# Kernel optimization log

Hardware: AMD Instinct MI355X
Metric: run time of the kernel (lower is better)

Reference implementation:

```python
import jax, jax.numpy as jnp
import numpy as np

N = 50000      # nodes per graph batch (per side)
E = 600000     # edges per side
B = 4096       # number of graphs (drug pairs)
D = 128        # node_dim == hidden_dim
K = 128        # kge_dim
R = 86         # rel_total
L = 3          # n_iter
EPS = 1e-5


def setup_inputs() -> dict:
    key = jax.random.key(0)
    ks = jax.random.split(key, 16)
    inp = {}
    inp["x1"] = jax.random.normal(ks[0], (N, D), jnp.float32)
    inp["x2"] = jax.random.normal(ks[1], (N, D), jnp.float32)
    inp["edge_index1"] = jax.random.randint(ks[2], (2, E), 0, N)
    inp["edge_index2"] = jax.random.randint(ks[3], (2, E), 0, N)
    inp["batch1"] = jnp.sort(jax.random.randint(ks[4], (N,), 0, B))
    inp["batch2"] = jnp.sort(jax.random.randint(ks[5], (N,), 0, B))
    inp["rel"] = jax.random.randint(ks[6], (B,), 0, R)
    # SAGEConv params, stacked over L layers (all [D,D] since node_dim==hidden_dim)
    sc = 0.05
    inp["Wl"] = jax.random.normal(ks[7], (L, D, D), jnp.float32) * sc   # lin on aggregated neighbors (has bias)
    inp["bl"] = jnp.zeros((L, D), jnp.float32)
    inp["Wr"] = jax.random.normal(ks[8], (L, D, D), jnp.float32) * sc   # root (self) lin, no bias
    # BatchNorm (eval mode: running stats)
    inp["bn_gamma"] = jnp.ones((L, D), jnp.float32)
    inp["bn_beta"] = jnp.zeros((L, D), jnp.float32)
    inp["bn_mean"] = jnp.zeros((L, D), jnp.float32)
    inp["bn_var"] = jnp.ones((L, D), jnp.float32)
    # relation embedding + final MLP
    inp["kge"] = jax.random.normal(ks[9], (R, K), jnp.float32)
    inp["W1"] = jax.random.normal(ks[10], (2 * D + K, D), jnp.float32) * sc
    inp["b1"] = jnp.zeros((D,), jnp.float32)
    inp["W2"] = jax.random.normal(ks[11], (D, 1), jnp.float32) * sc
    inp["b2"] = jnp.zeros((1,), jnp.float32)
    return inp


def _gnn(x, edge_index, Wl, bl, Wr, g, b, m, v):
    src, dst = edge_index[0], edge_index[1]
    deg = jax.ops.segment_sum(jnp.ones((E,), x.dtype), dst, num_segments=N)
    deg = jnp.maximum(deg, 1.0)[:, None]
    for i in range(L):
        agg = jax.ops.segment_sum(x[src], dst, num_segments=N) / deg  # mean aggregation
        h = agg @ Wl[i] + bl[i] + x @ Wr[i]                           # SAGEConv
        h = (h - m[i]) * (g[i] / jnp.sqrt(v[i] + EPS)) + b[i]         # BN (eval)
        x = jax.nn.relu(h)                                            # dropout = identity (eval)
    return x


def reference(x1, edge_index1, batch1, x2, edge_index2, batch2, rel,
              Wl, bl, Wr, bn_gamma, bn_beta, bn_mean, bn_var,
              kge, W1, b1, W2, b2):
    h1 = _gnn(x1, edge_index1, Wl, bl, Wr, bn_gamma, bn_beta, bn_mean, bn_var)
    h2 = _gnn(x2, edge_index2, Wl, bl, Wr, bn_gamma, bn_beta, bn_mean, bn_var)
    p1 = jax.ops.segment_sum(h1, batch1, num_segments=B)  # global_add_pool
    p2 = jax.ops.segment_sum(h2, batch2, num_segments=B)
    r = kge[rel]                                          # [B, K]
    z = jnp.concatenate([p1, p2, r], axis=-1)             # [B, 2D+K]
    h = jax.nn.relu(z @ W1 + b1)
    out = h @ W2 + b2
    return out.reshape(-1)
```

## Files before the change

### kernel.cpp

```cpp
#include <hip/hip_runtime.h>

#define NN 50000
#define NE 600000
#define NB 4096
#define DD 128
#define EPSV 1e-5f
#define NBKT 196
#define NCHUNK 256
#define CHSZ ((NE + NCHUNK - 1) / NCHUNK)

typedef __bf16 bf16x8 __attribute__((ext_vector_type(8)));
typedef float f32x4 __attribute__((ext_vector_type(4)));
typedef float f32x2 __attribute__((ext_vector_type(2)));

__device__ inline unsigned short f2bf(float f) {
    unsigned u = __float_as_uint(f);
    u = (u + 0x7FFFu + ((u >> 16) & 1u)) >> 16;
    return (unsigned short)u;
}
__device__ inline float bf2f(unsigned short h) {
    return __uint_as_float(((unsigned)h) << 16);
}

__global__ void k_prep(const float* __restrict__ x1, const float* __restrict__ x2,
                       unsigned short* __restrict__ xh, unsigned short* __restrict__ xl,
                       const float* __restrict__ Wl, const float* __restrict__ Wr,
                       const float* __restrict__ W1,
                       unsigned short* __restrict__ wfp, unsigned* __restrict__ w1p,
                       const int* __restrict__ d0, const int* __restrict__ d1,
                       int* __restrict__ bcnt) {
    __shared__ int h[NBKT];
    int b = blockIdx.x;
    int tid = threadIdx.x;
    if (b < 12500) {
        int i = b * 256 + tid;
        const float* x = (i < NN * 32) ? x1 : x2;
        int j = (i < NN * 32) ? i : i - NN * 32;
        float4 v = ((const float4*)x)[j];
        ushort4 hh, ll;
        hh.x = f2bf(v.x); ll.x = f2bf(v.x - bf2f(hh.x));
        hh.y = f2bf(v.y); ll.y = f2bf(v.y - bf2f(hh.y));
        hh.z = f2bf(v.z); ll.z = f2bf(v.z - bf2f(hh.z));
        hh.w = f2bf(v.w); ll.w = f2bf(v.w - bf2f(hh.w));
        ((ushort4*)xh)[i] = hh;
        ((ushort4*)xl)[i] = ll;
    } else if (b < 12500 + 576) {
        int t = (b - 12500) * 256 + tid;
        if (t < 3 * 128 * 256) {
            int k = t & 255;
            int n = (t >> 8) & 127;
            int l = t >> 15;
            float w = (k < 128) ? Wl[l * 16384 + k * 128 + n] : Wr[l * 16384 + (k - 128) * 128 + n];
            unsigned short hh = f2bf(w);
            unsigned short lo = f2bf(w - bf2f(hh));
            int c = k >> 5, kk = k & 31;
            size_t base = (size_t)l * 65536 + (size_t)c * 8192 + n * 32 + kk;
            wfp[base] = hh;
            wfp[base + 4096] = lo;
        } else if (t < 3 * 128 * 256 + 128 * 384) {
            int u = t - 3 * 128 * 256;
            int n = u / 384;
            int k = u - n * 384;
            float w = W1[k * 128 + n];
            unsigned short hh = f2bf(w);
            unsigned short ll = f2bf(w - bf2f(hh));
            w1p[u] = ((unsigned)hh << 16) | (unsigned)ll;
        }
    } else {
        int hb = b - 13076;
        int side = (hb >= NCHUNK) ? 1 : 0;
        int c = hb - side * NCHUNK;
        const int* dst = side ? d1 : d0;
        for (int i = tid; i < NBKT; i += 256) h[i] = 0;
        __syncthreads();
        int e0 = c * CHSZ, e1 = min(e0 + CHSZ, NE);
        for (int e = e0 + tid; e < e1; e += 256) atomicAdd(&h[dst[e] >> 8], 1);
        __syncthreads();
        int* bc = bcnt + ((size_t)side * NCHUNK + c) * NBKT;
        for (int i = tid; i < NBKT; i += 256) bc[i] = h[i];
    }
}

__global__ void k_s1(int* __restrict__ bcnt, int* __restrict__ btot) {
    int side = (blockIdx.x >= NBKT) ? 1 : 0;
    int b = blockIdx.x - side * NBKT;
    int tid = threadIdx.x;
    int idx = ((size_t)side * NCHUNK + tid) * NBKT + b;
    int v = bcnt[idx];
    int lane = tid & 63, wv = tid >> 6;
    int x = v;
#pragma unroll
    for (int off = 1; off < 64; off <<= 1) {
        int y = __shfl_up(x, off, 64);
        if (lane >= off) x += y;
    }
    __shared__ int ws4[4];
    if (lane == 63) ws4[wv] = x;
    __syncthreads();
    int add = 0;
#pragma unroll
    for (int w = 0; w < 4; w++)
        if (w < wv) add += ws4[w];
    int incl = x + add;
    bcnt[idx] = incl - v;
    if (tid == 255) btot[side * NBKT + b] = incl;
}

__global__ void k_s2(const int* __restrict__ btot, int* __restrict__ bbase,
                     int* __restrict__ ptrC) {
    int side = blockIdx.x;
    int tid = threadIdx.x;
    int v = (tid < NBKT) ? btot[side * NBKT + tid] : 0;
    int lane = tid & 63, wv = tid >> 6;
    int x = v;
#pragma unroll
    for (int off = 1; off < 64; off <<= 1) {
        int y = __shfl_up(x, off, 64);
        if (lane >= off) x += y;
    }
    __shared__ int ws4[4];
    if (lane == 63) ws4[wv] = x;
    __syncthreads();
    int add = 0;
#pragma unroll
    for (int w = 0; w < 4; w++)
        if (w < wv) add += ws4[w];
    int incl = x + add;
    if (tid < NBKT) bbase[side * NBKT + tid] = incl - v;
    if (tid == 0 && side == 1) ptrC[2 * NN] = 2 * NE;
}

__global__ void k_part(const int* __restrict__ s0, const int* __restrict__ d0,
                       const int* __restrict__ s1, const int* __restrict__ d1,
                       const int* __restrict__ bcnt, const int* __restrict__ bbase,
                       int* __restrict__ part) {
    int side = (blockIdx.x >= NCHUNK) ? 1 : 0;
    int c = blockIdx.x - side * NCHUNK;
    const int* src = side ? s1 : s0;
    const int* dst = side ? d1 : d0;
    int tid = threadIdx.x;
    __shared__ int off[NBKT];
    const int* bc = bcnt + ((size_t)side * NCHUNK + c) * NBKT;
    for (int i = tid; i < NBKT; i += 256) off[i] = bbase[side * NBKT + i] + bc[i];
    __syncthreads();
    int e0 = c * CHSZ, e1 = min(e0 + CHSZ, NE);
    int* P = part + (size_t)side * NE;
    int soff = side * NN;
    for (int e = e0 + tid; e < e1; e += 256) {
        int d = dst[e];
        int pos = atomicAdd(&off[d >> 8], 1);
        P[pos] = ((src[e] + soff) << 8) | (d & 255);
    }
}

__global__ void k_csr(const int* __restrict__ part, const int* __restrict__ bbase,
                      int* __restrict__ ptrC, float* __restrict__ invdC,
                      int* __restrict__ csrC) {
    int side = (blockIdx.x >= NBKT) ? 1 : 0;
    int b = blockIdx.x - side * NBKT;
    int tid = threadIdx.x;
    const int* P = part + (size_t)side * NE;
    int base = bbase[side * NBKT + b];
    int endp = (b == NBKT - 1) ? NE : bbase[side * NBKT + b + 1];
    __shared__ int cnt[256];
    cnt[tid] = 0;
    __syncthreads();
    for (int e = base + tid; e < endp; e += 256) atomicAdd(&cnt[P[e] & 255], 1);
    __syncthreads();
    int v = cnt[tid];
    int lane = tid & 63, wv = tid >> 6;
    int x = v;
#pragma unroll
    for (int off = 1; off < 64; off <<= 1) {
        int y = __shfl_up(x, off, 64);
        if (lane >= off) x += y;
    }
    __shared__ int ws4[4];
    if (lane == 63) ws4[wv] = x;
    __syncthreads();
    int add = 0;
#pragma unroll
    for (int w = 0; w < 4; w++)
        if (w < wv) add += ws4[w];
    int excl = x + add - v;
    int node = (b << 8) + tid;
    if (node < NN) {
        ptrC[side * NN + node] = side * NE + base + excl;
        invdC[side * NN + node] = 1.0f / (float)(v > 1 ? v : 1);
    }
    __syncthreads();
    cnt[tid] = excl;
    __syncthreads();
    for (int e = base + tid; e < endp; e += 256) {
        int p = P[e];
        int pos = atomicAdd(&cnt[p & 255], 1);
        csrC[(size_t)side * NE + base + pos] = p >> 8;
    }
}

__global__ void k_gather(const unsigned short* __restrict__ xh, const int* __restrict__ ptr,
                         const int* __restrict__ csr, const float* __restrict__ invd,
                         unsigned short* __restrict__ aggH) {
    int wid = threadIdx.x >> 6;
    int lane = threadIdx.x & 63;
    int q = lane >> 4;
    int c = lane & 15;
    int n = blockIdx.x * 4 + wid;
    if (n >= 2 * NN) return;
    int beg = ptr[n], end = ptr[n + 1];
    float id = invd[n];
    f32x2 a2[4];
#pragma unroll
    for (int k = 0; k < 4; k++) a2[k] = (f32x2){0.f, 0.f};

    for (int base = beg; base < end; base += 64) {
        int cnt = min(end - base, 64);
        int idxv = csr[base + min(lane, cnt - 1)];
        for (int e0 = 0; e0 < cnt; e0 += 8) {
            int eA = e0 + q;
            int eB = e0 + 4 + q;
            int iA = __shfl(idxv, eA, 64);
            int iB = __shfl(idxv, eB, 64);
            f32x2 wA2 = (eA < cnt) ? (f32x2){1.f, 1.f} : (f32x2){0.f, 0.f};
            f32x2 wB2 = (eB < cnt) ? (f32x2){1.f, 1.f} : (f32x2){0.f, 0.f};
            uint4 vA = *(const uint4*)(xh + (((unsigned)iA << 7) + (c << 3)));
            uint4 vB = *(const uint4*)(xh + (((unsigned)iB << 7) + (c << 3)));
            a2[0] += wA2 * (f32x2){__uint_as_float(vA.x << 16), __uint_as_float(vA.x & 0xffff0000u)};
            a2[1] += wA2 * (f32x2){__uint_as_float(vA.y << 16), __uint_as_float(vA.y & 0xffff0000u)};
            a2[2] += wA2 * (f32x2){__uint_as_float(vA.z << 16), __uint_as_float(vA.z & 0xffff0000u)};
            a2[3] += wA2 * (f32x2){__uint_as_float(vA.w << 16), __uint_as_float(vA.w & 0xffff0000u)};
            a2[0] += wB2 * (f32x2){__uint_as_float(vB.x << 16), __uint_as_float(vB.x & 0xffff0000u)};
            a2[1] += wB2 * (f32x2){__uint_as_float(vB.y << 16), __uint_as_float(vB.y & 0xffff0000u)};
            a2[2] += wB2 * (f32x2){__uint_as_float(vB.z << 16), __uint_as_float(vB.z & 0xffff0000u)};
            a2[3] += wB2 * (f32x2){__uint_as_float(vB.w << 16), __uint_as_float(vB.w & 0xffff0000u)};
        }
    }
    float a[8];
    a[0] = a2[0][0]; a[1] = a2[0][1];
    a[2] = a2[1][0]; a[3] = a2[1][1];
    a[4] = a2[2][0]; a[5] = a2[2][1];
    a[6] = a2[3][0]; a[7] = a2[3][1];
#pragma unroll
    for (int k = 0; k < 8; k++) {
        a[k] += __shfl_xor(a[k], 16, 64);
        a[k] += __shfl_xor(a[k], 32, 64);
    }
    if (q == 0) {
        unsigned short h0 = f2bf(a[0] * id), h1 = f2bf(a[1] * id);
        unsigned short h2 = f2bf(a[2] * id), h3 = f2bf(a[3] * id);
        unsigned short h4 = f2bf(a[4] * id), h5 = f2bf(a[5] * id);
        unsigned short h6 = f2bf(a[6] * id), h7 = f2bf(a[7] * id);
        uint4 o;
        o.x = (unsigned)h0 | ((unsigned)h1 << 16);
        o.y = (unsigned)h2 | ((unsigned)h3 << 16);
        o.z = (unsigned)h4 | ((unsigned)h5 << 16);
        o.w = (unsigned)h6 | ((unsigned)h7 << 16);
        *(uint4*)(aggH + (size_t)n * DD + c * 8) = o;
    }
}

__launch_bounds__(256)
__global__ void k_gemmL(const unsigned short* __restrict__ AH,
                        const unsigned short* __restrict__ XH, const unsigned short* __restrict__ XL,
                        const unsigned short* __restrict__ wfp,
                        const float* __restrict__ bl, const float* __restrict__ g,
                        const float* __restrict__ be, const float* __restrict__ mn,
                        const float* __restrict__ vr,
                        unsigned short* __restrict__ OH, unsigned short* __restrict__ OL,
                        float* __restrict__ Of, int f32out) {
    __shared__ __align__(16) unsigned short sA[2][128 * 32];
    __shared__ __align__(16) unsigned short sW[2][128 * 32];
    int tid = threadIdx.x;
    int lane = tid & 63, w = tid >> 6;
    int fm = lane & 15, kq = lane >> 4;
    int m0 = blockIdx.x * 128;
    int wr = (w & 1) * 64;
    int wn = (w >> 1) * 64;
    int ksw = kq ^ ((fm >> 1) & 3);

    int ldsoff[2], sfull[2];
    size_t gbase[2];
    bool sok[2];
#pragma unroll
    for (int i = 0; i < 2; i++) {
        int s = tid + 256 * i;
        int row = s >> 2, seg = s & 3;
        sfull[i] = s;
        ldsoff[i] = row * 32 + (seg ^ ((row >> 1) & 3)) * 8;
        int grow = m0 + row;
        sok[i] = grow < 2 * NN;
        gbase[i] = (size_t)grow * DD + seg * 8;
    }

    uint4 ph[2], plr[2], pwh[2], pwl[2];
#pragma unroll
    for (int i = 0; i < 2; i++) {
        ph[i] = sok[i] ? *(const uint4*)(AH + gbase[i]) : make_uint4(0, 0, 0, 0);
        pwh[i] = *(const uint4*)(wfp + sfull[i] * 8);
        pwl[i] = *(const uint4*)(wfp + 4096 + sfull[i] * 8);
    }

    float scv[4], shv[4];
#pragma unroll
    for (int nt = 0; nt < 4; nt++) {
        int jj = wn + nt * 16 + fm;
        float s = g[jj] * rsqrtf(vr[jj] + EPSV);
        scv[nt] = s;
        shv[nt] = (bl[jj] - mn[jj]) * s + be[jj];
    }

    f32x4 acc[4][4];
#pragma unroll
    for (int i = 0; i < 4; i++)
#pragma unroll
        for (int j = 0; j < 4; j++) acc[i][j] = (f32x4){0.f, 0.f, 0.f, 0.f};

#pragma unroll
    for (int c = 0; c < 8; c++) {
        int isA = (c < 4);
        if (c > 0) __syncthreads();
#pragma unroll
        for (int i = 0; i < 2; i++) {
            *(uint4*)&sA[0][ldsoff[i]] = ph[i];
            if (!isA) *(uint4*)&sA[1][ldsoff[i]] = plr[i];
            *(uint4*)&sW[0][ldsoff[i]] = pwh[i];
            *(uint4*)&sW[1][ldsoff[i]] = pwl[i];
        }
        if (c < 7) {
            int cn = c + 1;
            const unsigned short* SH = (cn < 4) ? AH : XH;
            size_t koff = (size_t)(cn & 3) * 32;
            const unsigned short* wbn = wfp + (size_t)cn * 8192;
#pragma unroll
            for (int i = 0; i < 2; i++) {
                ph[i] = sok[i] ? *(const uint4*)(SH + gbase[i] + koff) : make_uint4(0, 0, 0, 0);
                if (cn >= 4)
                    plr[i] = sok[i] ? *(const uint4*)(XL + gbase[i] + koff) : make_uint4(0, 0, 0, 0);
                pwh[i] = *(const uint4*)(wbn + sfull[i] * 8);
                pwl[i] = *(const uint4*)(wbn + 4096 + sfull[i] * 8);
            }
        }
        __syncthreads();

        bf16x8 ah[4], al[4];
#pragma unroll
        for (int mt = 0; mt < 4; mt++) {
            int r = wr + mt * 16 + fm;
            ah[mt] = *(const bf16x8*)&sA[0][r * 32 + ksw * 8];
            if (!isA) al[mt] = *(const bf16x8*)&sA[1][r * 32 + ksw * 8];
        }
#pragma unroll
        for (int nt = 0; nt < 4; nt++) {
            int nr = wn + nt * 16 + fm;
            bf16x8 wh = *(const bf16x8*)&sW[0][nr * 32 + ksw * 8];
            bf16x8 wl = *(const bf16x8*)&sW[1][nr * 32 + ksw * 8];
#pragma unroll
            for (int mt = 0; mt < 4; mt++) {
                acc[mt][nt] = __builtin_amdgcn_mfma_f32_16x16x32_bf16(ah[mt], wh, acc[mt][nt], 0, 0, 0);
                acc[mt][nt] = __builtin_amdgcn_mfma_f32_16x16x32_bf16(ah[mt], wl, acc[mt][nt], 0, 0, 0);
                if (!isA)
                    acc[mt][nt] = __builtin_amdgcn_mfma_f32_16x16x32_bf16(al[mt], wh, acc[mt][nt], 0, 0, 0);
            }
        }
    }

#pragma unroll
    for (int mt = 0; mt < 4; mt++) {
#pragma unroll
        for (int r = 0; r < 4; r++) {
            int grow = m0 + wr + mt * 16 + kq * 4 + r;
            if (grow < 2 * NN) {
#pragma unroll
                for (int nt = 0; nt < 4; nt++) {
                    int gcol = wn + nt * 16 + fm;
                    float o = fmaxf(acc[mt][nt][r] * scv[nt] + shv[nt], 0.f);
                    if (f32out) {
                        Of[(size_t)grow * DD + gcol] = o;
                    } else {
                        unsigned short h = f2bf(o);
                        OH[(size_t)grow * DD + gcol] = h;
                        OL[(size_t)grow * DD + gcol] = f2bf(o - bf2f(h));
                    }
                }
            }
        }
    }
}

__launch_bounds__(128)
__global__ void k_pool2z(const float* __restrict__ cf, const int* __restrict__ bt1,
                         const int* __restrict__ bt2, const int* __restrict__ rel,
                         const float* __restrict__ kge,
                         unsigned short* __restrict__ zh, unsigned short* __restrict__ zl) {
    int side = (blockIdx.x >= NB) ? 1 : 0;
    int b = blockIdx.x - side * NB;
    const int* batch = side ? bt2 : bt1;
    const float* h = cf + (size_t)side * NN * DD;
    __shared__ int sr[2];
    if (threadIdx.x < 2) {
        int target = b + (int)threadIdx.x;
        int lo = 0, hi = NN;
        while (lo < hi) {
            int mid = (lo + hi) >> 1;
            if (batch[mid] < target) lo = mid + 1; else hi = mid;
        }
        sr[threadIdx.x] = lo;
    }
    __syncthreads();
    int beg = sr[0], end = sr[1];
    int t = threadIdx.x;
    float acc = 0.f;
    for (int r = beg; r < end; r++) acc += h[(size_t)r * DD + t];
    size_t zo = (size_t)b * 384 + side * 128 + t;
    unsigned short hh = f2bf(acc);
    zh[zo] = hh;
    zl[zo] = f2bf(acc - bf2f(hh));
    if (side == 0) {
        float kv = kge[(size_t)rel[b] * 128 + t];
        size_t zk = (size_t)b * 384 + 256 + t;
        unsigned short kh = f2bf(kv);
        zh[zk] = kh;
        zl[zk] = f2bf(kv - bf2f(kh));
    }
}

__launch_bounds__(256)
__global__ void k_mlp2(const unsigned short* __restrict__ zh, const unsigned short* __restrict__ zl,
                       const unsigned* __restrict__ w1p,
                       const float* __restrict__ b1, const float* __restrict__ W2,
                       const float* __restrict__ b2, float* __restrict__ out) {
    __shared__ __align__(16) unsigned short sZ[2][32 * 40];
    __shared__ __align__(16) unsigned short sW[2][128 * 40];
    __shared__ float hpart[32][4];
    int tid = threadIdx.x;
    int m0 = blockIdx.x * 32;
    int lane = tid & 63, w = tid >> 6;
    int fm = lane & 15, q = lane >> 4;
    int wn = w * 32;

    f32x4 acc[2][2];
#pragma unroll
    for (int i = 0; i < 2; i++)
#pragma unroll
        for (int j = 0; j < 2; j++) acc[i][j] = (f32x4){0.f, 0.f, 0.f, 0.f};

    for (int c = 0; c < 12; c++) {
        int k0 = c * 32;
        __syncthreads();
        {
            int row = tid >> 3, seg = tid & 7;
            size_t off = (size_t)(m0 + row) * 384 + k0 + seg * 4;
            *(ushort4*)&sZ[0][row * 40 + seg * 4] = *(const ushort4*)(zh + off);
            *(ushort4*)&sZ[1][row * 40 + seg * 4] = *(const ushort4*)(zl + off);
        }
#pragma unroll
        for (int i = 0; i < 4; i++) {
            int u = tid + 256 * i;
            int row = u >> 3, seg = u & 7;
            uint4 val = *(const uint4*)(w1p + (size_t)row * 384 + k0 + seg * 4);
            ushort4 hi, lo;
            hi.x = val.x >> 16; hi.y = val.y >> 16; hi.z = val.z >> 16; hi.w = val.w >> 16;
            lo.x = val.x & 0xFFFF; lo.y = val.y & 0xFFFF; lo.z = val.z & 0xFFFF; lo.w = val.w & 0xFFFF;
            *(ushort4*)&sW[0][row * 40 + seg * 4] = hi;
            *(ushort4*)&sW[1][row * 40 + seg * 4] = lo;
        }
        __syncthreads();
        bf16x8 zfh[2], zfl[2];
#pragma unroll
        for (int mt = 0; mt < 2; mt++) {
            int r = mt * 16 + fm;
            zfh[mt] = *(const bf16x8*)&sZ[0][r * 40 + q * 8];
            zfl[mt] = *(const bf16x8*)&sZ[1][r * 40 + q * 8];
        }
#pragma unroll
        for (int nt = 0; nt < 2; nt++) {
            int nr = wn + nt * 16 + fm;
            bf16x8 wh = *(const bf16x8*)&sW[0][nr * 40 + q * 8];
            bf16x8 wl = *(const bf16x8*)&sW[1][nr * 40 + q * 8];
#pragma unroll
            for (int mt = 0; mt < 2; mt++) {
                acc[mt][nt] = __builtin_amdgcn_mfma_f32_16x16x32_bf16(zfh[mt], wh, acc[mt][nt], 0, 0, 0);
                acc[mt][nt] = __builtin_amdgcn_mfma_f32_16x16x32_bf16(zfh[mt], wl, acc[mt][nt], 0, 0, 0);
                acc[mt][nt] = __builtin_amdgcn_mfma_f32_16x16x32_bf16(zfl[mt], wh, acc[mt][nt], 0, 0, 0);
            }
        }
    }

    float b1v[2], w2v[2];
#pragma unroll
    for (int nt = 0; nt < 2; nt++) {
        int col = wn + nt * 16 + fm;
        b1v[nt] = b1[col];
        w2v[nt] = W2[col];
    }
#pragma unroll
    for (int mt = 0; mt < 2; mt++) {
#pragma unroll
        for (int r = 0; r < 4; r++) {
            float val = 0.f;
#pragma unroll
            for (int nt = 0; nt < 2; nt++)
                val += fmaxf(acc[mt][nt][r] + b1v[nt], 0.f) * w2v[nt];
#pragma unroll
            for (int m = 1; m < 16; m <<= 1) val += __shfl_xor(val, m, 64);
            if (fm == 0) hpart[mt * 16 + q * 4 + r][w] = val;
        }
    }
    __syncthreads();
    if (tid < 32)
        out[m0 + tid] = hpart[tid][0] + hpart[tid][1] + hpart[tid][2] + hpart[tid][3] + b2[0];
}

extern "C" void kernel_launch(void* const* d_in, const int* in_sizes, int n_in,
                              void* d_out, int out_size, void* d_ws, size_t ws_size,
                              hipStream_t stream) {
    const float* x1  = (const float*)d_in[0];
    const float* x2  = (const float*)d_in[1];
    const int*   ei1 = (const int*)d_in[2];
    const int*   ei2 = (const int*)d_in[3];
    const int*   bt1 = (const int*)d_in[4];
    const int*   bt2 = (const int*)d_in[5];
    const int*   rel = (const int*)d_in[6];
    const float* Wl  = (const float*)d_in[7];
    const float* bl  = (const float*)d_in[8];
    const float* Wr  = (const float*)d_in[9];
    const float* g   = (const float*)d_in[10];
    const float* be  = (const float*)d_in[11];
    const float* mn  = (const float*)d_in[12];
    const float* vr  = (const float*)d_in[13];
    const float* kge = (const float*)d_in[14];
    const float* W1  = (const float*)d_in[15];
    const float* b1v = (const float*)d_in[16];
    const float* W2  = (const float*)d_in[17];
    const float* b2v = (const float*)d_in[18];

    char* ws = (char*)d_ws;
    size_t off = 0;
    auto alloc = [&](size_t bytes) {
        void* p = ws + off;
        off += (bytes + 255) & ~(size_t)255;
        return p;
    };
    const size_t PL = (size_t)2 * NN * DD;
    unsigned short* xbufH = (unsigned short*)alloc(PL * 2);
    unsigned short* xbufL = (unsigned short*)alloc(PL * 2);
    unsigned short* obufH = (unsigned short*)alloc(PL * 2);
    unsigned short* obufL = (unsigned short*)alloc(PL * 2);
    unsigned short* aggH  = (unsigned short*)alloc(PL * 2);
    unsigned short* wfp   = (unsigned short*)alloc((size_t)3 * 65536 * 2);
    unsigned* w1p  = (unsigned*)alloc((size_t)128 * 384 * 4);
    unsigned short* zh = (unsigned short*)alloc((size_t)NB * 384 * 2);
    unsigned short* zl = (unsigned short*)alloc((size_t)NB * 384 * 2);
    int*   bcnt    = (int*)alloc((size_t)2 * NCHUNK * NBKT * 4);
    int*   btot    = (int*)alloc((size_t)2 * NBKT * 4);
    int*   bbase   = (int*)alloc((size_t)2 * NBKT * 4);
    int*   part    = (int*)alloc((size_t)2 * NE * 4);
    int*   ptrC    = (int*)alloc((size_t)(2 * NN + 1) * 4);
    float* invdC   = (float*)alloc((size_t)2 * NN * 4);
    int*   csrC    = (int*)alloc((size_t)2 * NE * 4);
    if (off > ws_size) return;

    float* cf = (float*)obufH;

    const int nbPrep  = 12500 + 576 + 512;
    const int nbNode4 = (2 * NN + 3) / 4;
    const int nbGemmL = (2 * NN + 127) / 128;

    k_prep<<<nbPrep, 256, 0, stream>>>(x1, x2, xbufH, xbufL, Wl, Wr, W1, wfp, w1p,
                                       ei1 + NE, ei2 + NE, bcnt);

    k_s1<<<2 * NBKT, 256, 0, stream>>>(bcnt, btot);
    k_s2<<<2, 256, 0, stream>>>(btot, bbase, ptrC);
    k_part<<<2 * NCHUNK, 256, 0, stream>>>(ei1, ei1 + NE, ei2, ei2 + NE, bcnt, bbase, part);
    k_csr<<<2 * NBKT, 256, 0, stream>>>(part, bbase, ptrC, invdC, csrC);

    k_gather<<<nbNode4, 256, 0, stream>>>(xbufH, ptrC, csrC, invdC, aggH);
    k_gemmL<<<nbGemmL, 256, 0, stream>>>(aggH, xbufH, xbufL, wfp, bl, g, be, mn, vr,
                                         obufH, obufL, (float*)nullptr, 0);
    k_gather<<<nbNode4, 256, 0, stream>>>(obufH, ptrC, csrC, invdC, aggH);
    k_gemmL<<<nbGemmL, 256, 0, stream>>>(aggH, obufH, obufL, wfp + 65536, bl + 128, g + 128,
                                         be + 128, mn + 128, vr + 128,
                                         xbufH, xbufL, (float*)nullptr, 0);
    k_gather<<<nbNode4, 256, 0, stream>>>(xbufH, ptrC, csrC, invdC, aggH);
    k_gemmL<<<nbGemmL, 256, 0, stream>>>(aggH, xbufH, xbufL, wfp + 131072, bl + 256, g + 256,
                                         be + 256, mn + 256, vr + 256,
                                         (unsigned short*)nullptr, (unsigned short*)nullptr, cf, 1);

    k_pool2z<<<2 * NB, 128, 0, stream>>>(cf, bt1, bt2, rel, kge, zh, zl);
    k_mlp2<<<NB / 32, 256, 0, stream>>>(zh, zl, w1p, b1v, W2, b2v, (float*)d_out);
}
```

Before: 493.7 us.

## Stage GEMM epilogue through LDS for coalesced stores; drop register prefetch

The GEMM epilogue now writes the activated results into shared memory in two halves and then stores them to global memory as 16-byte coalesced vectors, instead of scattered 2-byte or 4-byte per-lane stores. The bf16 hi/lo pair is packed into one word in LDS and split when it is written out. The register-level prefetch of the next K-chunk is also removed, and the K loop is no longer unrolled. Loads now happen right before the LDS stores, which lowers register pressure but loses the overlap of global loads with the MFMA work.

```diff
diff --git a/kernel.cpp b/kernel.cpp
--- a/kernel.cpp
+++ b/kernel.cpp
@@ -268,8 +268,9 @@
                         const float* __restrict__ vr,
                         unsigned short* __restrict__ OH, unsigned short* __restrict__ OL,
                         float* __restrict__ Of, int f32out) {
-    __shared__ __align__(16) unsigned short sA[2][128 * 32];
-    __shared__ __align__(16) unsigned short sW[2][128 * 32];
+    __shared__ __align__(16) unsigned short sBuf[4][128 * 32];
+    unsigned short (*sA)[128 * 32] = &sBuf[0];
+    unsigned short (*sW)[128 * 32] = &sBuf[2];
     int tid = threadIdx.x;
     int lane = tid & 63, w = tid >> 6;
     int fm = lane & 15, kq = lane >> 4;
@@ -278,28 +279,6 @@
     int wn = (w >> 1) * 64;
     int ksw = kq ^ ((fm >> 1) & 3);
 
-    int ldsoff[2], sfull[2];
-    size_t gbase[2];
-    bool sok[2];
-#pragma unroll
-    for (int i = 0; i < 2; i++) {
-        int s = tid + 256 * i;
-        int row = s >> 2, seg = s & 3;
-        sfull[i] = s;
-        ldsoff[i] = row * 32 + (seg ^ ((row >> 1) & 3)) * 8;
-        int grow = m0 + row;
-        sok[i] = grow < 2 * NN;
-        gbase[i] = (size_t)grow * DD + seg * 8;
-    }
-
-    uint4 ph[2], plr[2], pwh[2], pwl[2];
-#pragma unroll
-    for (int i = 0; i < 2; i++) {
-        ph[i] = sok[i] ? *(const uint4*)(AH + gbase[i]) : make_uint4(0, 0, 0, 0);
-        pwh[i] = *(const uint4*)(wfp + sfull[i] * 8);
-        pwl[i] = *(const uint4*)(wfp + 4096 + sfull[i] * 8);
-    }
-
     float scv[4], shv[4];
 #pragma unroll
     for (int nt = 0; nt < 4; nt++) {
@@ -315,30 +294,26 @@
 #pragma unroll
         for (int j = 0; j < 4; j++) acc[i][j] = (f32x4){0.f, 0.f, 0.f, 0.f};
 
-#pragma unroll
     for (int c = 0; c < 8; c++) {
         int isA = (c < 4);
         if (c > 0) __syncthreads();
+        const unsigned short* wb = wfp + (size_t)c * 8192;
 #pragma unroll
         for (int i = 0; i < 2; i++) {
-            *(uint4*)&sA[0][ldsoff[i]] = ph[i];
-            if (!isA) *(uint4*)&sA[1][ldsoff[i]] = plr[i];
-            *(uint4*)&sW[0][ldsoff[i]] = pwh[i];
-            *(uint4*)&sW[1][ldsoff[i]] = pwl[i];
-        }
-        if (c < 7) {
-            int cn = c + 1;
-            const unsigned short* SH = (cn < 4) ? AH : XH;
-            size_t koff = (size_t)(cn & 3) * 32;
-            const unsigned short* wbn = wfp + (size_t)cn * 8192;
-#pragma unroll
-            for (int i = 0; i < 2; i++) {
-                ph[i] = sok[i] ? *(const uint4*)(SH + gbase[i] + koff) : make_uint4(0, 0, 0, 0);
-                if (cn >= 4)
-                    plr[i] = sok[i] ? *(const uint4*)(XL + gbase[i] + koff) : make_uint4(0, 0, 0, 0);
-                pwh[i] = *(const uint4*)(wbn + sfull[i] * 8);
-                pwl[i] = *(const uint4*)(wbn + 4096 + sfull[i] * 8);
+            int s = tid + 256 * i;
+            int row = s >> 2, seg = s & 3;
+            int lo_ = row * 32 + ((seg ^ ((row >> 1) & 3)) << 3);
+            int grow = m0 + row;
+            size_t gofs = (size_t)grow * DD + (c & 3) * 32 + seg * 8;
+            uint4 av = make_uint4(0, 0, 0, 0), lv = make_uint4(0, 0, 0, 0);
+            if (grow < 2 * NN) {
+                av = *(const uint4*)((isA ? AH : XH) + gofs);
+                if (!isA) lv = *(const uint4*)(XL + gofs);
             }
+            *(uint4*)&sA[0][lo_] = av;
+            if (!isA) *(uint4*)&sA[1][lo_] = lv;
+            *(uint4*)&sW[0][lo_] = *(const uint4*)(wb + s * 8);
+            *(uint4*)&sW[1][lo_] = *(const uint4*)(wb + 4096 + s * 8);
         }
         __syncthreads();
 
@@ -364,23 +339,60 @@
         }
     }
 
-#pragma unroll
-    for (int mt = 0; mt < 4; mt++) {
-#pragma unroll
-        for (int r = 0; r < 4; r++) {
-            int grow = m0 + wr + mt * 16 + kq * 4 + r;
-            if (grow < 2 * NN) {
-#pragma unroll
-                for (int nt = 0; nt < 4; nt++) {
-                    int gcol = wn + nt * 16 + fm;
-                    float o = fmaxf(acc[mt][nt][r] * scv[nt] + shv[nt], 0.f);
-                    if (f32out) {
-                        Of[(size_t)grow * DD + gcol] = o;
-                    } else {
-                        unsigned short h = f2bf(o);
-                        OH[(size_t)grow * DD + gcol] = h;
-                        OL[(size_t)grow * DD + gcol] = f2bf(o - bf2f(h));
+    unsigned* cb = (unsigned*)sBuf;
+    int c8 = tid & 15;
+    for (int h = 0; h < 2; h++) {
+        __syncthreads();
+        if ((w & 1) == h) {
+#pragma unroll
+            for (int mt = 0; mt < 4; mt++) {
+#pragma unroll
+                for (int r = 0; r < 4; r++) {
+                    int rh = mt * 16 + kq * 4 + r;
+#pragma unroll
+                    for (int nt = 0; nt < 4; nt++) {
+                        int col = wn + nt * 16 + fm;
+                        float o = fmaxf(acc[mt][nt][r] * scv[nt] + shv[nt], 0.f);
+                        unsigned pv;
+                        if (f32out) {
+                            pv = __float_as_uint(o);
+                        } else {
+                            unsigned short hi_ = f2bf(o);
+                            pv = ((unsigned)hi_ << 16) | (unsigned)f2bf(o - bf2f(hi_));
+                        }
+                        cb[rh * 128 + col] = pv;
                     }
+                }
+            }
+        }
+        __syncthreads();
+        if (f32out) {
+#pragma unroll
+            for (int j = 0; j < 8; j++) {
+                int row = (tid >> 5) + j * 8;
+                int grow = m0 + h * 64 + row;
+                if (grow < 2 * NN)
+                    *(uint4*)&Of[(size_t)grow * DD + (tid & 31) * 4] =
+                        *(const uint4*)&cb[row * 128 + (tid & 31) * 4];
+            }
+        } else {
+#pragma unroll
+            for (int j = 0; j < 4; j++) {
+                int row = (tid >> 4) + j * 16;
+                int grow = m0 + h * 64 + row;
+                if (grow < 2 * NN) {
+                    const unsigned* u = &cb[row * 128 + c8 * 8];
+                    uint4 hv, lv2;
+                    hv.x = (u[0] >> 16) | (u[1] & 0xFFFF0000u);
+                    hv.y = (u[2] >> 16) | (u[3] & 0xFFFF0000u);
+                    hv.z = (u[4] >> 16) | (u[5] & 0xFFFF0000u);
+                    hv.w = (u[6] >> 16) | (u[7] & 0xFFFF0000u);
+                    lv2.x = (u[0] & 0xFFFFu) | (u[1] << 16);
+                    lv2.y = (u[2] & 0xFFFFu) | (u[3] << 16);
+                    lv2.z = (u[4] & 0xFFFFu) | (u[5] << 16);
+                    lv2.w = (u[6] & 0xFFFFu) | (u[7] << 16);
+                    *(uint4*)&OH[(size_t)grow * DD + c8 * 8] = hv;
+                    *(uint4*)&OL[(size_t)grow * DD + c8 * 8] = lv2;
                 }
             }
         }
```

After: 445.0 us. -9.9%, faster.
